# Kernel optimization log

Measured on AMD Instinct MI355X. Metric: run time of the kernel, lower is better.

## Reference

```python
import jax, jax.numpy as jnp
import numpy as np

B, N, C, H, W = 8, 512, 3, 16, 16
K, P, E = 2, 4, 1           # K: hop levels == filter taps, P: attn heads, E: edge feature sets
SLOPE = 0.2                 # LeakyReLU slope in attention
GAT_DIMS = {'d0': (128, 128), 'd1': (512, 32), 'u0': (128, 64),
            'u1': (256, 128), 's0': (128, 128), 's1': (512, 64)}


def _conv(x, w, b):
    pad = w.shape[-1] // 2
    y = jax.lax.conv_general_dilated(x, w, (1, 1), [(pad, pad), (pad, pad)],
                                     dimension_numbers=('NCHW', 'OIHW', 'NCHW'))
    return y + b[None, :, None, None]


def _gat(x, S, wk, wq, wf, b):
    # x: (B,G,N); S: (B,E,N,N) binary GSO. KeyQuery attention + K-tap attentional filter.
    key = jnp.einsum('pegf,bgn->bpefn', wk, x)
    qry = jnp.einsum('pegf,bgn->bpefn', wq, x)
    # scores[...,n,m]: logit of node n attending to neighbor m
    scores = jax.nn.leaky_relu(jnp.einsum('bpefn,bpefm->bpenm', qry, key), SLOPE)
    mask = (jnp.abs(S) > 1e-9)[:, None]                    # (B,1,E,N,N)
    aij = jnp.where(mask, jax.nn.softmax(jnp.where(mask, scores, -1e9), axis=-1), 0.0)
    Pn, En, Kt, G, F = wf.shape
    xk = jnp.broadcast_to(x[:, None, None], (x.shape[0], Pn, En, G, x.shape[-1]))
    zs = [xk]
    for _ in range(Kt - 1):
        xk = jnp.einsum('bpegm,bpenm->bpegn', xk, aij)     # attention-weighted diffusion
        zs.append(xk)
    z = jnp.stack(zs, axis=3)                              # (B,P,E,K,G,N)
    y = jnp.einsum('bpekgn,pekgf->bpfn', z, wf) + b[None, None, :, None]
    y = jax.nn.relu(y)                                     # nonlinearity before head concat
    return y.reshape(y.shape[0], Pn * F, y.shape[-1])      # (B, P*F, N)


def _forward(x, Slist, conv0_w, conv0_b, conv1_w, conv1_b, flat_w, flat_b,
             d0_wk, d0_wq, d0_wf, d0_b, d1_wk, d1_wq, d1_wf, d1_b,
             u0_wk, u0_wq, u0_wf, u0_b, u1_wk, u1_wq, u1_wf, u1_b,
             s0_wk, s0_wq, s0_wf, s0_b, s1_wk, s1_wq, s1_wf, s1_b,
             dec0_w, dec0_b, dec1_w, dec1_b):
    Bn, Nn = x.shape[0], x.shape[1]
    h = x.reshape(Bn * Nn, C, H, W)
    e = jax.nn.relu(_conv(h, conv0_w, conv0_b))
    e = jax.nn.relu(_conv(e, conv1_w, conv1_b))
    e = e + h                                              # RES connection after encoder
    f = jax.nn.relu(e.reshape(Bn * Nn, -1) @ flat_w.T + flat_b)
    g = f.reshape(Bn, -1, Nn)                              # faithful torch reshape to (B, F, N)
    S0, S1 = Slist[:, 0:1], Slist[:, 1:2]
    p0 = g
    p1 = _gat(p0, S0, d0_wk, d0_wq, d0_wf, d0_b)           # downward pass
    p2 = _gat(p1, S1, d1_wk, d1_wq, d1_wf, d1_b)
    # upward pass + shortcuts (upward[l] uses S[K-l-1]; shortcut[K-1-l] on p[K-1-l])
    u0 = _gat(p2, S1, u0_wk, u0_wq, u0_wf, u0_b) + _gat(p1, S1, s1_wk, s1_wq, s1_wf, s1_b)
    u1 = _gat(u0, S0, u1_wk, u1_wq, u1_wf, u1_b) + _gat(p0, S0, s0_wk, s0_wq, s0_wf, s0_b)
    d = jax.nn.relu(u1.reshape(Bn * Nn, -1) @ dec0_w.T + dec0_b)
    out = jax.nn.softmax(d @ dec1_w.T + dec1_b, axis=-1)   # nn.Softmax() -> dim=1 on 2D input
    return out.reshape(Bn, Nn, -1)


def setup_inputs() -> dict:
    key = jax.random.key(0)
    ks = iter(jax.random.split(key, 64))
    def nrm(shape, s=0.1):
        return jax.random.normal(next(ks), shape, jnp.float32) * s
    x = jax.random.normal(next(ks), (B, N, C, H, W), jnp.float32)
    adj = (jax.random.uniform(next(ks), (B, K, N, N)) < 0.02).astype(jnp.float32)
    Slist = jnp.clip(adj + jnp.eye(N, dtype=jnp.float32)[None, None], 0.0, 1.0)
    inp = {'x': x, 'Slist': Slist,
           'conv0_w': nrm((32, C, 3, 3)), 'conv0_b': nrm((32,)),
           'conv1_w': nrm((C, 32, 3, 3)), 'conv1_b': nrm((C,)),
           'flat_w': nrm((128, C * H * W)), 'flat_b': nrm((128,))}
    for pre, (G, F) in GAT_DIMS.items():
        inp[pre + '_wk'] = nrm((P, E, G, F))
        inp[pre + '_wq'] = nrm((P, E, G, F))
        inp[pre + '_wf'] = nrm((P, E, K, G, F))
        inp[pre + '_b'] = nrm((F,))
    inp.update({'dec0_w': nrm((256, 512)), 'dec0_b': nrm((256,)),
                'dec1_w': nrm((5, 256)), 'dec1_b': nrm((5,))})
    return inp


def reference(x, Slist, conv0_w, conv0_b, conv1_w, conv1_b, flat_w, flat_b,
              d0_wk, d0_wq, d0_wf, d0_b, d1_wk, d1_wq, d1_wf, d1_b,
              u0_wk, u0_wq, u0_wf, u0_b, u1_wk, u1_wq, u1_wf, u1_b,
              s0_wk, s0_wq, s0_wf, s0_b, s1_wk, s1_wq, s1_wf, s1_b,
              dec0_w, dec0_b, dec1_w, dec1_b):
    return _forward(x, Slist, conv0_w, conv0_b, conv1_w, conv1_b, flat_w, flat_b,
                    d0_wk, d0_wq, d0_wf, d0_b, d1_wk, d1_wq, d1_wf, d1_b,
                    u0_wk, u0_wq, u0_wf, u0_b, u1_wk, u1_wq, u1_wf, u1_b,
                    s0_wk, s0_wq, s0_wf, s0_b, s1_wk, s1_wq, s1_wf, s1_b,
                    dec0_w, dec0_b, dec1_w, dec1_b)
```

## Files before the change

### kernel.cpp

```cpp
#include <hip/hip_runtime.h>
#include <hip/hip_bf16.h>
#include <math.h>

typedef unsigned short u16;
typedef unsigned int   u32;

#define CAP 48

__device__ __forceinline__ float tof(u16 u){
  union { u32 i; float f; } v; v.i = ((u32)u) << 16; return v.f;
}
__device__ __forceinline__ u16 fromf(float f){
  union { float f; u32 i; } v; v.f = f;
  u32 x = v.i;
  return (u16)((x + 0x7fffu + ((x >> 16) & 1u)) >> 16);
}

__global__ void detect_dtype(const void* xp, int* flag){
  if(threadIdx.x == 0 && blockIdx.x == 0){
    const u16* p = (const u16*)xp;
    int outl = 0;
    for(int i = 0; i < 128; i++){
      u16 u = p[2*i];
      int e = (u >> 7) & 0xFF;
      if(u != 0 && (e < 100 || e > 140)) outl++;
    }
    *flag = (outl > 32) ? 1 : 0;
  }
}

struct WArgs {
  const void* p[34];
  int sz[34];
  int off[35];
};

__global__ __launch_bounds__(256) void convert_weights(WArgs wa, const int* flag,
                                                       float* __restrict__ arena, int total){
  int i = blockIdx.x * 256 + threadIdx.x;
  if(i >= total) return;
  int isf = *flag;
  int t = 0;
  while(wa.off[t+1] <= i) t++;
  int j = i - wa.off[t];
  float v = 0.f;
  if(j < wa.sz[t])
    v = isf ? ((const float*)wa.p[t])[j] : tof(((const u16*)wa.p[t])[j]);
  arena[i] = v;
}

__global__ __launch_bounds__(256) void transpose_w(const float* __restrict__ src,
                                                   float* __restrict__ dst, int R, int C){
  int i = blockIdx.x * 256 + threadIdx.x;
  if(i < R*C){
    int r = i / C, c = i - r*C;
    dst[(size_t)c*R + r] = src[i];
  }
}

__global__ __launch_bounds__(64) void build_nbr(const void* __restrict__ S,
                                                int* __restrict__ nbr_idx,
                                                int* __restrict__ nbr_cnt,
                                                const int* __restrict__ flag){
  int isf = *flag;
  int row  = blockIdx.x;
  int lane = threadIdx.x;
  int cnt = 0;
  for(int c = 0; c < 8; c++){
    int m = c*64 + lane;
    size_t idx = (size_t)row * 512 + m;
    float sv = isf ? ((const float*)S)[idx] : tof(((const u16*)S)[idx]);
    bool pred = fabsf(sv) > 1e-9f;
    unsigned long long mask = __ballot(pred);
    int pos = cnt + __popcll(mask & ((1ull << lane) - 1ull));
    if(pred && pos < CAP) nbr_idx[(size_t)row*CAP + pos] = m;
    cnt += __popcll(mask);
  }
  if(lane == 0) nbr_cnt[row] = cnt > CAP ? CAP : cnt;
}

__global__ __launch_bounds__(256) void encoder_conv(
    const void* __restrict__ x, const int* __restrict__ flag,
    const float* __restrict__ w0, const float* __restrict__ b0,
    const float* __restrict__ w1, const float* __restrict__ b1,
    float* __restrict__ e1n)
{
  __shared__ float xpad[3][18][18];
  __shared__ float e0p[16][18][18];

  int isf = *flag;
  int tid = threadIdx.x;
  size_t img = blockIdx.x;
  int py = tid >> 4, px = tid & 15;

  float* z1 = &xpad[0][0][0];
  for(int i = tid; i < 972; i += 256) z1[i] = 0.f;
  float* z2 = &e0p[0][0][0];
  for(int i = tid; i < 5184; i += 256) z2[i] = 0.f;
  __syncthreads();

  #pragma unroll
  for(int i = 0; i < 3; i++){
    size_t gi = img*768 + i*256 + tid;
    xpad[i][1+py][1+px] = isf ? ((const float*)x)[gi] : tof(((const u16*)x)[gi]);
  }
  __syncthreads();

  float acc1[3] = {0.f, 0.f, 0.f};

  for(int grp = 0; grp < 2; grp++){
    float acc0[16];
    #pragma unroll
    for(int o = 0; o < 16; o++) acc0[o] = 0.f;
    for(int i = 0; i < 3; i++){
      float rr[9];
      #pragma unroll
      for(int ky = 0; ky < 3; ky++)
        #pragma unroll
        for(int kx = 0; kx < 3; kx++)
          rr[ky*3+kx] = xpad[i][py+ky][px+kx];
      #pragma unroll
      for(int o = 0; o < 16; o++){
        #pragma unroll
        for(int t = 0; t < 9; t++)
          acc0[o] = fmaf(rr[t], w0[(grp*16+o)*27 + i*9 + t], acc0[o]);
      }
    }
    __syncthreads();
    #pragma unroll
    for(int o = 0; o < 16; o++)
      e0p[o][1+py][1+px] = fmaxf(acc0[o] + b0[grp*16 + o], 0.f);
    __syncthreads();

    for(int i = 0; i < 16; i++){
      float rr[9];
      #pragma unroll
      for(int ky = 0; ky < 3; ky++)
        #pragma unroll
        for(int kx = 0; kx < 3; kx++)
          rr[ky*3+kx] = e0p[i][py+ky][px+kx];
      int ic = grp*16 + i;
      #pragma unroll
      for(int o = 0; o < 3; o++){
        #pragma unroll
        for(int t = 0; t < 9; t++)
          acc1[o] = fmaf(rr[t], w1[o*288 + ic*9 + t], acc1[o]);
      }
    }
  }

  #pragma unroll
  for(int o = 0; o < 3; o++)
    e1n[img*768 + o*256 + tid] = fmaxf(acc1[o] + b1[o], 0.f) + xpad[o][1+py][1+px];
}

__global__ __launch_bounds__(256) void gemm_flat(
    const float* __restrict__ e1n, const float* __restrict__ fwT,
    const float* __restrict__ fb, float* __restrict__ g)
{
  __shared__ float As[16][68];
  __shared__ float Bs[16][68];
  int tid = threadIdx.x;
  int n0 = blockIdx.x * 64, m0 = blockIdx.y * 64;

  int lk = tid >> 4;
  int l4 = (tid & 15) * 4;
  int br = tid >> 2;
  int bc = (tid & 3) * 4;

  float acc[4][4];
  #pragma unroll
  for(int i = 0; i < 4; i++)
    #pragma unroll
    for(int jj = 0; jj < 4; jj++) acc[i][jj] = 0.f;

  int tm = tid >> 4, tn = tid & 15;
  for(int kt = 0; kt < 48; kt++){
    int k0 = kt*16;
    *(float4*)&As[lk][l4] = *(const float4*)&fwT[(size_t)(k0 + lk)*128 + m0 + l4];
    float4 bv = *(const float4*)&e1n[(size_t)(n0 + br)*768 + k0 + bc];
    Bs[bc+0][br] = bv.x; Bs[bc+1][br] = bv.y; Bs[bc+2][br] = bv.z; Bs[bc+3][br] = bv.w;
    __syncthreads();
    #pragma unroll
    for(int kk = 0; kk < 16; kk++){
      float4 a  = *(const float4*)&As[kk][tm*4];
      float4 xx = *(const float4*)&Bs[kk][tn*4];
      float av[4]  = {a.x, a.y, a.z, a.w};
      float xvv[4] = {xx.x, xx.y, xx.z, xx.w};
      #pragma unroll
      for(int i = 0; i < 4; i++)
        #pragma unroll
        for(int jj = 0; jj < 4; jj++)
          acc[i][jj] = fmaf(av[i], xvv[jj], acc[i][jj]);
    }
    __syncthreads();
  }

  #pragma unroll
  for(int jj = 0; jj < 4; jj++){
    int img = n0 + tn*4 + jj;
    float4 r = make_float4(fmaxf(acc[0][jj] + fb[m0+tm*4+0], 0.f),
                           fmaxf(acc[1][jj] + fb[m0+tm*4+1], 0.f),
                           fmaxf(acc[2][jj] + fb[m0+tm*4+2], 0.f),
                           fmaxf(acc[3][jj] + fb[m0+tm*4+3], 0.f));
    *(float4*)&g[(size_t)img*128 + m0 + tm*4] = r;
  }
}

struct KqP { const float* X; const float* wk; const float* wq; float* kqT;
             int G, F, my; };

__global__ __launch_bounds__(256) void gemm_kq2(KqP A, KqP B)
{
  __shared__ float Ws[32*68];
  __shared__ float Xs[32*68];
  int tid = threadIdx.x;
  int by = blockIdx.y;
  KqP P = (by < A.my) ? A : B;
  int lby = (by < A.my) ? by : (by - A.my);
  int bp = blockIdx.z;
  int b = bp >> 2, p = bp & 3;
  int n0 = blockIdx.x * 64, m0 = lby * 64;
  const float* Xb = P.X + (size_t)b * P.G * 512;

  int lk = tid >> 4;
  int l4 = (tid & 15) * 4;

  int mg = m0 + l4;
  int quad = mg / P.F;
  int mq = mg - quad * P.F;
  size_t GF = (size_t)P.G * P.F;
  const float* wb = (quad == 0 ? P.wk : P.wq) + (size_t)p * GF + mq;

  float acc[4][4];
  #pragma unroll
  for(int i = 0; i < 4; i++)
    #pragma unroll
    for(int jj = 0; jj < 4; jj++) acc[i][jj] = 0.f;

  int tm = tid >> 4, tn = tid & 15;
  int KT = P.G / 32;
  for(int kt = 0; kt < KT; kt++){
    int k = kt*32 + lk;
    *(float4*)&Ws[lk*68 + l4]      = *(const float4*)(wb + (size_t)k * P.F);
    *(float4*)&Ws[(lk+16)*68 + l4] = *(const float4*)(wb + (size_t)(k+16) * P.F);
    *(float4*)&Xs[lk*68 + l4]      = *(const float4*)(Xb + (size_t)k * 512 + n0 + l4);
    *(float4*)&Xs[(lk+16)*68 + l4] = *(const float4*)(Xb + (size_t)(k+16) * 512 + n0 + l4);
    __syncthreads();
    #pragma unroll
    for(int kk = 0; kk < 32; kk++){
      float4 a  = *(const float4*)&Ws[kk*68 + tm*4];
      float4 xx = *(const float4*)&Xs[kk*68 + tn*4];
      float av[4]  = {a.x, a.y, a.z, a.w};
      float xvv[4] = {xx.x, xx.y, xx.z, xx.w};
      #pragma unroll
      for(int i = 0; i < 4; i++)
        #pragma unroll
        for(int jj = 0; jj < 4; jj++)
          acc[i][jj] = fmaf(av[i], xvv[jj], acc[i][jj]);
    }
    __syncthreads();
  }

  int F2 = 2*P.F;
  float* ob = P.kqT + (size_t)bp * 512 * F2;
  #pragma unroll
  for(int jj = 0; jj < 4; jj++){
    float* orow = ob + (size_t)(n0 + tn*4 + jj) * F2 + m0 + tm*4;
    #pragma unroll
    for(int i = 0; i < 4; i++) orow[i] = acc[i][jj];
  }
}

__global__ __launch_bounds__(256) void gemm_kqK64(
    const float* __restrict__ X,
    const float* __restrict__ wk, const float* __restrict__ wq,
    float* __restrict__ kqT, int G, int F)
{
  __shared__ float Ws[64][68];
  __shared__ float Xs[64][68];
  int tid = threadIdx.x;
  int bp = blockIdx.z;
  int b = bp >> 2, p = bp & 3;
  int n0 = blockIdx.x * 64, m0 = blockIdx.y * 64;
  const float* Xb = X + (size_t)b * G * 512;

  int lk = tid >> 4;
  int l4 = (tid & 15) * 4;

  int mg = m0 + l4;
  int quad = mg / F;
  int mq = mg - quad * F;
  size_t GF = (size_t)G * F;
  const float* wb = (quad == 0 ? wk : wq) + (size_t)p * GF + mq;

  float acc[4][4];
  #pragma unroll
  for(int i = 0; i < 4; i++)
    #pragma unroll
    for(int jj = 0; jj < 4; jj++) acc[i][jj] = 0.f;

  int tm = tid >> 4, tn = tid & 15;
  int KT = G / 64;
  for(int kt = 0; kt < KT; kt++){
    #pragma unroll
    for(int kb = 0; kb < 4; kb++){
      int k = kt*64 + lk + kb*16;
      *(float4*)&Ws[lk + kb*16][l4] = *(const float4*)(wb + (size_t)k * F);
      *(float4*)&Xs[lk + kb*16][l4] = *(const float4*)(Xb + (size_t)k * 512 + n0 + l4);
    }
    __syncthreads();
    #pragma unroll
    for(int kk = 0; kk < 64; kk++){
      float4 a  = *(const float4*)&Ws[kk][tm*4];
      float4 xx = *(const float4*)&Xs[kk][tn*4];
      float av[4]  = {a.x, a.y, a.z, a.w};
      float xvv[4] = {xx.x, xx.y, xx.z, xx.w};
      #pragma unroll
      for(int i = 0; i < 4; i++)
        #pragma unroll
        for(int jj = 0; jj < 4; jj++)
          acc[i][jj] = fmaf(av[i], xvv[jj], acc[i][jj]);
    }
    __syncthreads();
  }

  int F2 = 2*F;
  float* ob = kqT + (size_t)bp * 512 * F2;
  #pragma unroll
  for(int jj = 0; jj < 4; jj++){
    float* orow = ob + (size_t)(n0 + tn*4 + jj) * F2 + m0 + tm*4;
    #pragma unroll
    for(int i = 0; i < 4; i++) orow[i] = acc[i][jj];
  }
}

struct AtP { const float* kqT; float* aijv; int F, s; };

__global__ __launch_bounds__(256) void attn2(
    AtP A, AtP B,
    const int* __restrict__ nbr_idx, const int* __restrict__ nbr_cnt)
{
  __shared__ float qs[16][132];
  __shared__ float sc[16][CAP];
  __shared__ float red[16][2];
  int tid = threadIdx.x;
  int n0 = blockIdx.x * 16;
  int bp = blockIdx.y;
  AtP P = (blockIdx.z == 0) ? A : B;
  int b = bp >> 2;
  int F = P.F;
  int F2 = 2*F;
  const float* kqT = P.kqT;

  int F4 = F >> 2;
  for(int i = tid; i < 16*F4; i += 256){
    int r = i / F4, c4 = (i - r*F4) * 4;
    *(float4*)&qs[r][c4] =
      *(const float4*)&kqT[((size_t)bp*512 + n0 + r)*F2 + F + c4];
  }
  __syncthreads();

  int r = tid >> 4;
  int t = tid & 15;
  int n = n0 + r;
  int srow = (b*2 + P.s)*512 + n;
  int cnt = nbr_cnt[srow];
  const int* il = nbr_idx + (size_t)srow * CAP;

  for(int j = t; j < cnt; j += 16){
    int m = il[j];
    const float* krow = kqT + ((size_t)bp*512 + m)*F2;
    float a = 0.f;
    for(int f = 0; f < F; f += 4){
      float4 k4 = *(const float4*)&krow[f];
      a = fmaf(qs[r][f],   k4.x, a);
      a = fmaf(qs[r][f+1], k4.y, a);
      a = fmaf(qs[r][f+2], k4.z, a);
      a = fmaf(qs[r][f+3], k4.w, a);
    }
    sc[r][j] = a >= 0.f ? a : 0.2f * a;
  }
  __syncthreads();

  if(t == 0){
    float mx = -1e30f;
    for(int j = 0; j < cnt; j++) mx = fmaxf(mx, sc[r][j]);
    float ssum = 0.f;
    for(int j = 0; j < cnt; j++) ssum += expf(sc[r][j] - mx);
    red[r][0] = mx; red[r][1] = ssum;
  }
  __syncthreads();

  float mx = red[r][0], ssum = red[r][1];
  float* arow = P.aijv + ((size_t)bp*512 + n)*CAP;
  for(int j = t; j < cnt; j += 16)
    arow[j] = expf(sc[r][j] - mx) / ssum;
}

struct FiP { const float* X; const float* aijv; float* Xp; int G, s, gy; };

__global__ __launch_bounds__(256) void fill_Xp2(
    FiP A, FiP B,
    const int* __restrict__ nbr_idx, const int* __restrict__ nbr_cnt)
{
  __shared__ float xrows[8][512];
  __shared__ float av_s[64][CAP+1];
  __shared__ u16   il_s[64][CAP+2];
  __shared__ int   cnt_s[64];

  int tid = threadIdx.x;
  int by = blockIdx.y;
  FiP P = (by < A.gy) ? A : B;
  int lby = (by < A.gy) ? by : (by - A.gy);
  int n0 = blockIdx.x * 64;
  int g0 = lby * 32;
  int bp = blockIdx.z;
  int b = bp >> 2;
  int srow0 = (b*2 + P.s)*512 + n0;

  for(int i = tid; i < 64*CAP; i += 256){
    int r = i / CAP, j = i - r*CAP;
    il_s[r][j] = (u16)nbr_idx[(size_t)(srow0 + r)*CAP + j];
    av_s[r][j] = P.aijv[((size_t)bp*512 + n0 + r)*CAP + j];
  }
  if(tid < 64) cnt_s[tid] = nbr_cnt[srow0 + tid];

  int n_l = tid & 63;
  int gs  = tid >> 6;
  const float* Xb  = P.X  + ((size_t)b  * P.G + g0) * 512;
  float*       XpB = P.Xp + ((size_t)bp * P.G + g0) * 512;

  for(int gb = 0; gb < 32; gb += 8){
    __syncthreads();
    for(int i = tid; i < 8*128; i += 256){
      int gr = i >> 7, c4 = (i & 127) * 4;
      *(float4*)&xrows[gr][c4] = *(const float4*)&Xb[(size_t)(gb + gr)*512 + c4];
    }
    __syncthreads();
    int cnt = cnt_s[n_l];
    float a0 = 0.f, a1 = 0.f;
    for(int j = 0; j < cnt; j++){
      float w = av_s[n_l][j];
      int   m = il_s[n_l][j];
      a0 = fmaf(w, xrows[gs][m],     a0);
      a1 = fmaf(w, xrows[gs + 4][m], a1);
    }
    XpB[(size_t)(gb + gs)*512     + n0 + n_l] = a0;
    XpB[(size_t)(gb + gs + 4)*512 + n0 + n_l] = a1;
  }
}

struct YP { const float* X; const float* Xp; const float* wf; const float* bias;
            float* out; int G, F, PF, acc, my; };

__global__ __launch_bounds__(256) void gemm_y2_32(YP A, YP B)
{
  __shared__ float Ws[32*68];
  __shared__ float Xs[32*68];
  int tid = threadIdx.x;
  int by = blockIdx.y;
  YP P = (by < A.my) ? A : B;
  int lby = (by < A.my) ? by : (by - A.my);
  int bp = blockIdx.z;
  int b = bp >> 2, p = bp & 3;
  int n0 = blockIdx.x * 64, m0 = lby * 64;
  int G = P.G, F = P.F;

  int lk = tid >> 4;
  int l4 = (tid & 15) * 4;
  int mg = m0 + l4;
  int fcl = mg < F ? mg : (F - 4);
  size_t GF2 = (size_t)2 * G * F;
  const float* wb = P.wf + (size_t)p * GF2 + fcl;

  float acc[4][4];
  #pragma unroll
  for(int i = 0; i < 4; i++)
    #pragma unroll
    for(int jj = 0; jj < 4; jj++) acc[i][jj] = 0.f;

  int tm = tid >> 4, tn = tid & 15;
  int KT = (2*G) / 32;
  for(int kt = 0; kt < KT; kt++){
    int c0 = kt*32 + lk;
    int c1 = c0 + 16;
    const float* xr0 = (c0 < G) ? (P.X  + ((size_t)b  * G + c0      ) * 512)
                                : (P.Xp + ((size_t)bp * G + (c0 - G)) * 512);
    const float* xr1 = (c1 < G) ? (P.X  + ((size_t)b  * G + c1      ) * 512)
                                : (P.Xp + ((size_t)bp * G + (c1 - G)) * 512);
    *(float4*)&Ws[lk*68 + l4]      = *(const float4*)(wb + (size_t)c0 * F);
    *(float4*)&Ws[(lk+16)*68 + l4] = *(const float4*)(wb + (size_t)c1 * F);
    *(float4*)&Xs[lk*68 + l4]      = *(const float4*)(xr0 + n0 + l4);
    *(float4*)&Xs[(lk+16)*68 + l4] = *(const float4*)(xr1 + n0 + l4);
    __syncthreads();
    #pragma unroll
    for(int kk = 0; kk < 32; kk++){
      float4 a  = *(const float4*)&Ws[kk*68 + tm*4];
      float4 xx = *(const float4*)&Xs[kk*68 + tn*4];
      float av[4]  = {a.x, a.y, a.z, a.w};
      float xvv[4] = {xx.x, xx.y, xx.z, xx.w};
      #pragma unroll
      for(int i = 0; i < 4; i++)
        #pragma unroll
        for(int jj = 0; jj < 4; jj++)
          acc[i][jj] = fmaf(av[i], xvv[jj], acc[i][jj]);
    }
    __syncthreads();
  }

  int mrow = m0 + tm*4;
  if(mrow < F){
    float* ob = P.out + ((size_t)b * P.PF + (size_t)p * F + mrow) * 512 + n0 + tn*4;
    #pragma unroll
    for(int i = 0; i < 4; i++){
      float bv = P.bias[mrow + i];
      float4 r = make_float4(fmaxf(acc[i][0] + bv, 0.f),
                             fmaxf(acc[i][1] + bv, 0.f),
                             fmaxf(acc[i][2] + bv, 0.f),
                             fmaxf(acc[i][3] + bv, 0.f));
      float* dst = ob + (size_t)i * 512;
      if(P.acc){
        float4 old = *(float4*)dst;
        r.x += old.x; r.y += old.y; r.z += old.z; r.w += old.w;
      }
      *(float4*)dst = r;
    }
  }
}

__global__ __launch_bounds__(256) void gemm_y2_K64(YP A, YP B)
{
  __shared__ float Ws[64*68];
  __shared__ float Xs[64*68];
  int tid = threadIdx.x;
  int by = blockIdx.y;
  YP P = (by < A.my) ? A : B;
  int lby = (by < A.my) ? by : (by - A.my);
  int bp = blockIdx.z;
  int b = bp >> 2, p = bp & 3;
  int n0 = blockIdx.x * 64, m0 = lby * 64;
  int G = P.G, F = P.F;

  int lk = tid >> 4;
  int l4 = (tid & 15) * 4;
  int mg = m0 + l4;
  int fcl = mg < F ? mg : (F - 4);
  size_t GF2 = (size_t)2 * G * F;
  const float* wb = P.wf + (size_t)p * GF2 + fcl;

  float acc[4][4];
  #pragma unroll
  for(int i = 0; i < 4; i++)
    #pragma unroll
    for(int jj = 0; jj < 4; jj++) acc[i][jj] = 0.f;

  int tm = tid >> 4, tn = tid & 15;
  int KT = (2*G) / 64;
  for(int kt = 0; kt < KT; kt++){
    #pragma unroll
    for(int kb = 0; kb < 4; kb++){
      int c = kt*64 + lk + kb*16;
      const float* xr = (c < G) ? (P.X  + ((size_t)b  * G + c      ) * 512)
                                : (P.Xp + ((size_t)bp * G + (c - G)) * 512);
      *(float4*)&Ws[(lk + kb*16)*68 + l4] = *(const float4*)(wb + (size_t)c * F);
      *(float4*)&Xs[(lk + kb*16)*68 + l4] = *(const float4*)(xr + n0 + l4);
    }
    __syncthreads();
    #pragma unroll
    for(int kk = 0; kk < 64; kk++){
      float4 a  = *(const float4*)&Ws[kk*68 + tm*4];
      float4 xx = *(const float4*)&Xs[kk*68 + tn*4];
      float av[4]  = {a.x, a.y, a.z, a.w};
      float xvv[4] = {xx.x, xx.y, xx.z, xx.w};
      #pragma unroll
      for(int i = 0; i < 4; i++)
        #pragma unroll
        for(int jj = 0; jj < 4; jj++)
          acc[i][jj] = fmaf(av[i], xvv[jj], acc[i][jj]);
    }
    __syncthreads();
  }

  int mrow = m0 + tm*4;
  if(mrow < F){
    float* ob = P.out + ((size_t)b * P.PF + (size_t)p * F + mrow) * 512 + n0 + tn*4;
    #pragma unroll
    for(int i = 0; i < 4; i++){
      float bv = P.bias[mrow + i];
      float4 r = make_float4(fmaxf(acc[i][0] + bv, 0.f),
                             fmaxf(acc[i][1] + bv, 0.f),
                             fmaxf(acc[i][2] + bv, 0.f),
                             fmaxf(acc[i][3] + bv, 0.f));
      float* dst = ob + (size_t)i * 512;
      if(P.acc){
        float4 old = *(float4*)dst;
        r.x += old.x; r.y += old.y; r.z += old.z; r.w += old.w;
      }
      *(float4*)dst = r;
    }
  }
}

__global__ __launch_bounds__(256) void add_vec(float* __restrict__ dst,
                                               const float* __restrict__ src, int n4){
  int i = blockIdx.x * 256 + threadIdx.x;
  if(i < n4){
    float4 a = ((const float4*)dst)[i];
    float4 b = ((const float4*)src)[i];
    a.x += b.x; a.y += b.y; a.z += b.z; a.w += b.w;
    ((float4*)dst)[i] = a;
  }
}

__global__ __launch_bounds__(256) void gemm_dec0(
    const float* __restrict__ u1, const float* __restrict__ w0T,
    const float* __restrict__ b0, float* __restrict__ d)
{
  __shared__ float As[16][68];
  __shared__ float Bs[16][68];
  int tid = threadIdx.x;
  int n0 = blockIdx.x * 64;
  int m0 = blockIdx.y * 64;

  int lk = tid >> 4;
  int l4 = (tid & 15) * 4;
  int br = tid >> 2;
  int bc = (tid & 3) * 4;

  float acc[4][4];
  #pragma unroll
  for(int i = 0; i < 4; i++)
    #pragma unroll
    for(int jj = 0; jj < 4; jj++) acc[i][jj] = 0.f;

  int tm = tid >> 4, tn = tid & 15;
  for(int kt = 0; kt < 32; kt++){
    int k0 = kt*16;
    *(float4*)&As[lk][l4] = *(const float4*)&w0T[(size_t)(k0 + lk)*256 + m0 + l4];
    float4 bv = *(const float4*)&u1[(size_t)(n0 + br)*512 + k0 + bc];
    Bs[bc+0][br] = bv.x; Bs[bc+1][br] = bv.y; Bs[bc+2][br] = bv.z; Bs[bc+3][br] = bv.w;
    __syncthreads();
    #pragma unroll
    for(int kk = 0; kk < 16; kk++){
      float4 a  = *(const float4*)&As[kk][tm*4];
      float4 xx = *(const float4*)&Bs[kk][tn*4];
      float av[4]  = {a.x, a.y, a.z, a.w};
      float xvv[4] = {xx.x, xx.y, xx.z, xx.w};
      #pragma unroll
      for(int i = 0; i < 4; i++)
        #pragma unroll
        for(int jj = 0; jj < 4; jj++)
          acc[i][jj] = fmaf(av[i], xvv[jj], acc[i][jj]);
    }
    __syncthreads();
  }

  #pragma unroll
  for(int jj = 0; jj < 4; jj++){
    int row = n0 + tn*4 + jj;
    float4 r = make_float4(fmaxf(acc[0][jj] + b0[m0+tm*4+0], 0.f),
                           fmaxf(acc[1][jj] + b0[m0+tm*4+1], 0.f),
                           fmaxf(acc[2][jj] + b0[m0+tm*4+2], 0.f),
                           fmaxf(acc[3][jj] + b0[m0+tm*4+3], 0.f));
    *(float4*)&d[(size_t)row*256 + m0 + tm*4] = r;
  }
}

__global__ __launch_bounds__(64) void decoder2(
    const float* __restrict__ d,
    const float* __restrict__ w1, const float* __restrict__ b1,
    const int* __restrict__ flag, void* __restrict__ outp)
{
  __shared__ float ds[256];
  __shared__ float lg[5];
  int r = blockIdx.x, lane = threadIdx.x;
  for(int i = lane; i < 256; i += 64) ds[i] = d[(size_t)r*256 + i];
  __syncthreads();

  if(lane < 5){
    float a = 0.f;
    const float* wr = w1 + (size_t)lane * 256;
    for(int i = 0; i < 256; i++) a = fmaf(ds[i], wr[i], a);
    lg[lane] = a + b1[lane];
  }
  __syncthreads();
  if(lane < 5){
    float mx = lg[0];
    for(int i = 1; i < 5; i++) mx = fmaxf(mx, lg[i]);
    float ssum = 0.f;
    for(int i = 0; i < 5; i++) ssum += expf(lg[i] - mx);
    float v = expf(lg[lane] - mx) / ssum;
    if(*flag) ((float*)outp)[(size_t)r*5 + lane] = v;
    else      ((u16*)outp)[(size_t)r*5 + lane] = fromf(v);
  }
}

extern "C" void kernel_launch(void* const* d_in, const int* in_sizes, int n_in,
                              void* d_out, int out_size, void* d_ws, size_t ws_size,
                              hipStream_t stream)
{
  (void)n_in; (void)out_size; (void)ws_size;
  const void* x = d_in[0];
  const void* S = d_in[1];

  float* wsf   = (float*)d_ws;
  int*   flag  = (int*)d_ws;
  float* arena = wsf + 1024;

  WArgs wa;
  long long aoff[35]; aoff[0] = 0;
  for(int t = 0; t < 34; t++){
    wa.p[t]  = d_in[2 + t];
    wa.sz[t] = in_sizes[2 + t];
    wa.off[t] = (int)aoff[t];
    aoff[t+1] = aoff[t] + ((in_sizes[2 + t] + 15) & ~15);
  }
  wa.off[34] = (int)aoff[34];
  int total = (int)aoff[34];

  size_t cur = 1024 + (size_t)((total + 1023) & ~1023);
  float* g    = wsf + cur; cur += 524288;
  float* p1   = wsf + cur; cur += 2097152;
  float* p2   = wsf + cur; cur += 524288;
  float* u0b  = wsf + cur; cur += 1048576;
  float* u0c  = wsf + cur; cur += 1048576;
  float* u1c  = wsf + cur; cur += 2097152;
  float* u1b  = p1;
  float* aijvA= wsf + cur; cur += (size_t)32*512*CAP;
  float* aijvB= wsf + cur; cur += (size_t)32*512*CAP;
  float* fwT  = wsf + cur; cur += 98304;
  float* dw0T = wsf + cur; cur += 131072;
  int*   ncnt = (int*)(wsf + cur); cur += 8192;
  int*   nidx = (int*)(wsf + cur); cur += (size_t)8192 * CAP;
  float* pool = wsf + cur; cur += 10485760;

  float* e1n   = pool;
  float* kqT0  = pool;
  float* Xp0   = pool;
  float* kqT1  = pool;
  float* Xp1   = pool;
  float* kqT2  = pool;
  float* kqT3  = pool + 2097152;
  float* Xp2   = pool;
  float* Xp3   = pool + 2097152;
  float* kqT4  = pool;
  float* kqT5  = pool + 4194304;
  float* Xp4   = pool;
  float* Xp5   = pool + 4194304;
  float* dbuf  = pool;

  const float* A[34];
  for(int t = 0; t < 34; t++) A[t] = arena + aoff[t];
  const float* c0w = A[0], *c0b = A[1], *c1w = A[2], *c1b = A[3];
  const float* fw  = A[4], *fb  = A[5];
  const float *wk_[6], *wq_[6], *wf_[6], *bias_[6];
  for(int l = 0; l < 6; l++){
    wk_[l]   = A[6 + 4*l];
    wq_[l]   = A[7 + 4*l];
    wf_[l]   = A[8 + 4*l];
    bias_[l] = A[9 + 4*l];
  }
  const float* dw0 = A[30], *db0 = A[31], *dw1 = A[32], *db1 = A[33];

  detect_dtype<<<1, 64, 0, stream>>>(x, flag);
  convert_weights<<<(total + 255)/256, 256, 0, stream>>>(wa, flag, arena, total);
  transpose_w<<<(98304 + 255)/256, 256, 0, stream>>>(fw, fwT, 128, 768);
  transpose_w<<<(131072 + 255)/256, 256, 0, stream>>>(dw0, dw0T, 256, 512);
  build_nbr<<<8192, 64, 0, stream>>>(S, nidx, ncnt, flag);
  encoder_conv<<<4096, 256, 0, stream>>>(x, flag, c0w, c0b, c1w, c1b, e1n);
  gemm_flat<<<dim3(64, 2), 256, 0, stream>>>(e1n, fwT, fb, g);

  {
    KqP k0 = { g, wk_[0], wq_[0], kqT0, 128, 128, 4 };
    gemm_kq2<<<dim3(8, 4, 32), 256, 0, stream>>>(k0, k0);
    AtP a0 = { kqT0, aijvA, 128, 0 };
    attn2<<<dim3(32, 32, 1), 256, 0, stream>>>(a0, a0, nidx, ncnt);
    FiP f0 = { g, aijvA, Xp0, 128, 0, 4 };
    fill_Xp2<<<dim3(8, 4, 32), 256, 0, stream>>>(f0, f0, nidx, ncnt);
    YP y0 = { g, Xp0, wf_[0], bias_[0], p1, 128, 128, 512, 0, 2 };
    gemm_y2_32<<<dim3(8, 2, 32), 256, 0, stream>>>(y0, y0);
  }

  {
    gemm_kqK64<<<dim3(8, 1, 32), 256, 0, stream>>>(p1, wk_[1], wq_[1], kqT1, 512, 32);
    AtP a1 = { kqT1, aijvA, 32, 1 };
    attn2<<<dim3(32, 32, 1), 256, 0, stream>>>(a1, a1, nidx, ncnt);
    FiP f1 = { p1, aijvA, Xp1, 512, 1, 16 };
    fill_Xp2<<<dim3(8, 16, 32), 256, 0, stream>>>(f1, f1, nidx, ncnt);
    YP y1 = { p1, Xp1, wf_[1], bias_[1], p2, 512, 32, 128, 0, 1 };
    gemm_y2_K64<<<dim3(8, 1, 32), 256, 0, stream>>>(y1, y1);
  }

  {
    KqP k2 = { p2, wk_[2], wq_[2], kqT2, 128, 64, 2 };
    KqP k3 = { p1, wk_[5], wq_[5], kqT3, 512, 64, 2 };
    gemm_kq2<<<dim3(8, 4, 32), 256, 0, stream>>>(k2, k3);
    AtP a2 = { kqT2, aijvA, 64, 1 };
    AtP a3 = { kqT3, aijvB, 64, 1 };
    attn2<<<dim3(32, 32, 2), 256, 0, stream>>>(a2, a3, nidx, ncnt);
    FiP f2 = { p2, aijvA, Xp2, 128, 1, 4 };
    FiP f3 = { p1, aijvB, Xp3, 512, 1, 16 };
    fill_Xp2<<<dim3(8, 20, 32), 256, 0, stream>>>(f2, f3, nidx, ncnt);
    YP y2 = { p2, Xp2, wf_[2], bias_[2], u0b, 128, 64, 256, 0, 1 };
    YP y3 = { p1, Xp3, wf_[5], bias_[5], u0c, 512, 64, 256, 0, 1 };
    gemm_y2_K64<<<dim3(8, 2, 32), 256, 0, stream>>>(y2, y3);
    add_vec<<<1024, 256, 0, stream>>>(u0b, u0c, 262144);
  }

  {
    KqP k4 = { u0b, wk_[3], wq_[3], kqT4, 256, 128, 4 };
    KqP k5 = { g,   wk_[4], wq_[4], kqT5, 128, 128, 4 };
    gemm_kq2<<<dim3(8, 8, 32), 256, 0, stream>>>(k4, k5);
    AtP a4 = { kqT4, aijvA, 128, 0 };
    AtP a5 = { kqT5, aijvB, 128, 0 };
    attn2<<<dim3(32, 32, 2), 256, 0, stream>>>(a4, a5, nidx, ncnt);
    FiP f4 = { u0b, aijvA, Xp4, 256, 0, 8 };
    FiP f5 = { g,   aijvB, Xp5, 128, 0, 4 };
    fill_Xp2<<<dim3(8, 12, 32), 256, 0, stream>>>(f4, f5, nidx, ncnt);
    YP y4 = { u0b, Xp4, wf_[3], bias_[3], u1b, 256, 128, 512, 0, 2 };
    YP y5 = { g,   Xp5, wf_[4], bias_[4], u1c, 128, 128, 512, 0, 2 };
    gemm_y2_32<<<dim3(8, 4, 32), 256, 0, stream>>>(y4, y5);
    add_vec<<<2048, 256, 0, stream>>>(u1b, u1c, 524288);
  }

  gemm_dec0<<<dim3(64, 4), 256, 0, stream>>>(u1b, dw0T, db0, dbuf);
  decoder2<<<4096, 64, 0, stream>>>(dbuf, dw1, db1, flag, d_out);
}
```

Baseline: 961.2 us.

## Restructure sparse neighbor gather to map lanes over feature rows

The sparse attention-diffusion kernel now gives each group of 16 lanes one node, with every lane handling a different feature row. Neighbor weights and indices are interleaved in one shared control array, so the lanes of a node read the same entries as broadcasts. The per-block feature tile shrinks from 32 to 16 rows and is loaded once with padded rows, which doubles the grid. Results are staged in shared memory so the global writes are float4 and coalesced. The cost is more blocks that reload the same control data, plus lanes idling up to the largest neighbor count in the wavefront.

Result: slower. 1.302 ms (+35.5%).

```diff
diff --git a/kernel.cpp b/kernel.cpp
--- a/kernel.cpp
+++ b/kernel.cpp
@@ -400,13 +400,13 @@
 
 struct FiP { const float* X; const float* aijv; float* Xp; int G, s, gy; };
 
-__global__ __launch_bounds__(256) void fill_Xp2(
+__global__ __launch_bounds__(256) void fill_Xp3(
     FiP A, FiP B,
     const int* __restrict__ nbr_idx, const int* __restrict__ nbr_cnt)
 {
-  __shared__ float xrows[8][512];
-  __shared__ float av_s[64][CAP+1];
-  __shared__ u16   il_s[64][CAP+2];
+  __shared__ float xrows[16*514];
+  __shared__ u32   ctrl[64*98];
+  __shared__ float out_s[16*68];
   __shared__ int   cnt_s[64];
 
   int tid = threadIdx.x;
@@ -414,40 +414,67 @@
   FiP P = (by < A.gy) ? A : B;
   int lby = (by < A.gy) ? by : (by - A.gy);
   int n0 = blockIdx.x * 64;
-  int g0 = lby * 32;
+  int g0 = lby * 16;
   int bp = blockIdx.z;
   int b = bp >> 2;
   int srow0 = (b*2 + P.s)*512 + n0;
 
   for(int i = tid; i < 64*CAP; i += 256){
     int r = i / CAP, j = i - r*CAP;
-    il_s[r][j] = (u16)nbr_idx[(size_t)(srow0 + r)*CAP + j];
-    av_s[r][j] = P.aijv[((size_t)bp*512 + n0 + r)*CAP + j];
+    u32 wb = __float_as_uint(P.aijv[((size_t)bp*512 + n0 + r)*CAP + j]);
+    u32 mm = (u32)nbr_idx[(size_t)(srow0 + r)*CAP + j];
+    ctrl[r*98 + 2*j]     = wb;
+    ctrl[r*98 + 2*j + 1] = mm;
   }
   if(tid < 64) cnt_s[tid] = nbr_cnt[srow0 + tid];
 
-  int n_l = tid & 63;
-  int gs  = tid >> 6;
-  const float* Xb  = P.X  + ((size_t)b  * P.G + g0) * 512;
-  float*       XpB = P.Xp + ((size_t)bp * P.G + g0) * 512;
-
-  for(int gb = 0; gb < 32; gb += 8){
-    __syncthreads();
-    for(int i = tid; i < 8*128; i += 256){
-      int gr = i >> 7, c4 = (i & 127) * 4;
-      *(float4*)&xrows[gr][c4] = *(const float4*)&Xb[(size_t)(gb + gr)*512 + c4];
-    }
-    __syncthreads();
+  const float* Xb = P.X + ((size_t)b * P.G + g0) * 512;
+  for(int i = tid; i < 16*256; i += 256){
+    int gr = i >> 8, c2 = (i & 255) * 2;
+    float2 v = *(const float2*)&Xb[(size_t)gr*512 + c2];
+    *(float2*)&xrows[gr*514 + c2] = v;
+  }
+  __syncthreads();
+
+  int g_l  = tid & 15;
+  int slot = (tid >> 4) & 3;
+  int wv   = tid >> 6;
+
+  const float* xg = &xrows[g_l*514];
+
+  for(int it = 0; it < 4; it++){
+    int n_l = wv*16 + it*4 + slot;
     int cnt = cnt_s[n_l];
-    float a0 = 0.f, a1 = 0.f;
-    for(int j = 0; j < cnt; j++){
-      float w = av_s[n_l][j];
-      int   m = il_s[n_l][j];
-      a0 = fmaf(w, xrows[gs][m],     a0);
-      a1 = fmaf(w, xrows[gs + 4][m], a1);
-    }
-    XpB[(size_t)(gb + gs)*512     + n0 + n_l] = a0;
-    XpB[(size_t)(gb + gs + 4)*512 + n0 + n_l] = a1;
+    int jmax = cnt;
+    jmax = max(jmax, __shfl_xor(jmax, 16));
+    jmax = max(jmax, __shfl_xor(jmax, 32));
+    const u32* cn = &ctrl[n_l*98];
+    float acc = 0.f;
+    int j = 0;
+    for(; j + 2 <= jmax; j += 2){
+      u32 w0b = cn[2*j],   m0 = cn[2*j+1] & 511u;
+      u32 w1b = cn[2*j+2], m1 = cn[2*j+3] & 511u;
+      float w0 = (j   < cnt) ? __uint_as_float(w0b) : 0.f;
+      float w1 = (j+1 < cnt) ? __uint_as_float(w1b) : 0.f;
+      float x0 = xg[m0];
+      float x1 = xg[m1];
+      acc = fmaf(w0, x0, acc);
+      acc = fmaf(w1, x1, acc);
+    }
+    if(j < jmax){
+      u32 w0b = cn[2*j]; u32 m0 = cn[2*j+1] & 511u;
+      float w0 = (j < cnt) ? __uint_as_float(w0b) : 0.f;
+      acc = fmaf(w0, xg[m0], acc);
+    }
+    out_s[g_l*68 + n_l] = acc;
+  }
+  __syncthreads();
+
+  float* XpB = P.Xp + ((size_t)bp * P.G + g0) * 512;
+  {
+    int gr = tid >> 4, c4 = (tid & 15) * 4;
+    float4 v = *(float4*)&out_s[gr*68 + c4];
+    *(float4*)&XpB[(size_t)gr*512 + n0 + c4] = v;
   }
 }
 
@@ -776,8 +803,8 @@
     gemm_kq2<<<dim3(8, 4, 32), 256, 0, stream>>>(k0, k0);
     AtP a0 = { kqT0, aijvA, 128, 0 };
     attn2<<<dim3(32, 32, 1), 256, 0, stream>>>(a0, a0, nidx, ncnt);
-    FiP f0 = { g, aijvA, Xp0, 128, 0, 4 };
-    fill_Xp2<<<dim3(8, 4, 32), 256, 0, stream>>>(f0, f0, nidx, ncnt);
+    FiP f0 = { g, aijvA, Xp0, 128, 0, 8 };
+    fill_Xp3<<<dim3(8, 8, 32), 256, 0, stream>>>(f0, f0, nidx, ncnt);
     YP y0 = { g, Xp0, wf_[0], bias_[0], p1, 128, 128, 512, 0, 2 };
     gemm_y2_32<<<dim3(8, 2, 32), 256, 0, stream>>>(y0, y0);
   }
@@ -786,8 +813,8 @@
     gemm_kqK64<<<dim3(8, 1, 32), 256, 0, stream>>>(p1, wk_[1], wq_[1], kqT1, 512, 32);
     AtP a1 = { kqT1, aijvA, 32, 1 };
     attn2<<<dim3(32, 32, 1), 256, 0, stream>>>(a1, a1, nidx, ncnt);
-    FiP f1 = { p1, aijvA, Xp1, 512, 1, 16 };
-    fill_Xp2<<<dim3(8, 16, 32), 256, 0, stream>>>(f1, f1, nidx, ncnt);
+    FiP f1 = { p1, aijvA, Xp1, 512, 1, 32 };
+    fill_Xp3<<<dim3(8, 32, 32), 256, 0, stream>>>(f1, f1, nidx, ncnt);
     YP y1 = { p1, Xp1, wf_[1], bias_[1], p2, 512, 32, 128, 0, 1 };
     gemm_y2_K64<<<dim3(8, 1, 32), 256, 0, stream>>>(y1, y1);
   }
@@ -799,9 +826,9 @@
     AtP a2 = { kqT2, aijvA, 64, 1 };
     AtP a3 = { kqT3, aijvB, 64, 1 };
     attn2<<<dim3(32, 32, 2), 256, 0, stream>>>(a2, a3, nidx, ncnt);
-    FiP f2 = { p2, aijvA, Xp2, 128, 1, 4 };
-    FiP f3 = { p1, aijvB, Xp3, 512, 1, 16 };
-    fill_Xp2<<<dim3(8, 20, 32), 256, 0, stream>>>(f2, f3, nidx, ncnt);
+    FiP f2 = { p2, aijvA, Xp2, 128, 1, 8 };
+    FiP f3 = { p1, aijvB, Xp3, 512, 1, 32 };
+    fill_Xp3<<<dim3(8, 40, 32), 256, 0, stream>>>(f2, f3, nidx, ncnt);
     YP y2 = { p2, Xp2, wf_[2], bias_[2], u0b, 128, 64, 256, 0, 1 };
     YP y3 = { p1, Xp3, wf_[5], bias_[5], u0c, 512, 64, 256, 0, 1 };
     gemm_y2_K64<<<dim3(8, 2, 32), 256, 0, stream>>>(y2, y3);
@@ -815,9 +842,9 @@
     AtP a4 = { kqT4, aijvA, 128, 0 };
     AtP a5 = { kqT5, aijvB, 128, 0 };
     attn2<<<dim3(32, 32, 2), 256, 0, stream>>>(a4, a5, nidx, ncnt);
-    FiP f4 = { u0b, aijvA, Xp4, 256, 0, 8 };
-    FiP f5 = { g,   aijvB, Xp5, 128, 0, 4 };
-    fill_Xp2<<<dim3(8, 12, 32), 256, 0, stream>>>(f4, f5, nidx, ncnt);
+    FiP f4 = { u0b, aijvA, Xp4, 256, 0, 16 };
+    FiP f5 = { g,   aijvB, Xp5, 128, 0, 8 };
+    fill_Xp3<<<dim3(8, 24, 32), 256, 0, stream>>>(f4, f5, nidx, ncnt);
     YP y4 = { u0b, Xp4, wf_[3], bias_[3], u1b, 256, 128, 512, 0, 2 };
     YP y5 = { g,   Xp5, wf_[4], bias_[4], u1c, 128, 128, 512, 0, 2 };
     gemm_y2_32<<<dim3(8, 4, 32), 256, 0, stream>>>(y4, y5);
```

## Pack attention weight and neighbor index into u64 and restructure sparse diffusion

Applied to the files above, without the earlier changes.

The attention kernel now writes each softmax weight together with its neighbor index as a packed 64-bit control word, so the diffusion kernel no longer reloads the separate neighbor index table. The new fill kernel stages 16 feature rows transposed into shared memory (padded stride 18) and has each thread gather four features per neighbor with float2 loads, reading control words straight from global memory. The grid doubles along the feature axis to match the smaller per-block slice. The control buffer doubles in size, and the unrolled loop reads up to three padding entries past the neighbor count (masked to zero weight), which depends on the buffer tail being readable.

Measured after the change: 917.3 us. 1.05x faster.

```diff
diff --git a/kernel.cpp b/kernel.cpp
--- a/kernel.cpp
+++ b/kernel.cpp
@@ -4,6 +4,7 @@
 
 typedef unsigned short u16;
 typedef unsigned int   u32;
+typedef unsigned long long u64;
 
 #define CAP 48
 
@@ -335,7 +336,7 @@
   }
 }
 
-struct AtP { const float* kqT; float* aijv; int F, s; };
+struct AtP { const float* kqT; u64* ctrl; int F, s; };
 
 __global__ __launch_bounds__(256) void attn2(
     AtP A, AtP B,
@@ -393,62 +394,73 @@
   __syncthreads();
 
   float mx = red[r][0], ssum = red[r][1];
-  float* arow = P.aijv + ((size_t)bp*512 + n)*CAP;
-  for(int j = t; j < cnt; j += 16)
-    arow[j] = expf(sc[r][j] - mx) / ssum;
-}
-
-struct FiP { const float* X; const float* aijv; float* Xp; int G, s, gy; };
-
-__global__ __launch_bounds__(256) void fill_Xp2(
-    FiP A, FiP B,
-    const int* __restrict__ nbr_idx, const int* __restrict__ nbr_cnt)
-{
-  __shared__ float xrows[8][512];
-  __shared__ float av_s[64][CAP+1];
-  __shared__ u16   il_s[64][CAP+2];
-  __shared__ int   cnt_s[64];
+  u64* crow = P.ctrl + ((size_t)bp*512 + n)*CAP;
+  for(int j = t; j < cnt; j += 16){
+    float w = expf(sc[r][j] - mx) / ssum;
+    crow[j] = (u64)__float_as_uint(w) | ((u64)(u32)il[j] << 32);
+  }
+}
+
+struct FiP { const float* X; const u64* ctrl; float* Xp; int G, s, gy; };
+
+__global__ __launch_bounds__(256) void fill_Xp4(
+    FiP A, FiP B, const int* __restrict__ nbr_cnt)
+{
+  __shared__ float xi[512*18];
 
   int tid = threadIdx.x;
   int by = blockIdx.y;
   FiP P = (by < A.gy) ? A : B;
   int lby = (by < A.gy) ? by : (by - A.gy);
   int n0 = blockIdx.x * 64;
-  int g0 = lby * 32;
+  int g0 = lby * 16;
   int bp = blockIdx.z;
   int b = bp >> 2;
   int srow0 = (b*2 + P.s)*512 + n0;
 
-  for(int i = tid; i < 64*CAP; i += 256){
-    int r = i / CAP, j = i - r*CAP;
-    il_s[r][j] = (u16)nbr_idx[(size_t)(srow0 + r)*CAP + j];
-    av_s[r][j] = P.aijv[((size_t)bp*512 + n0 + r)*CAP + j];
-  }
-  if(tid < 64) cnt_s[tid] = nbr_cnt[srow0 + tid];
+  const float* Xb = P.X + ((size_t)b * P.G + g0) * 512;
+  for(int i = tid; i < 16*512; i += 256){
+    int gl = i >> 9, m = i & 511;
+    xi[m*18 + gl] = Xb[(size_t)gl*512 + m];
+  }
 
   int n_l = tid & 63;
-  int gs  = tid >> 6;
-  const float* Xb  = P.X  + ((size_t)b  * P.G + g0) * 512;
-  float*       XpB = P.Xp + ((size_t)bp * P.G + g0) * 512;
-
-  for(int gb = 0; gb < 32; gb += 8){
-    __syncthreads();
-    for(int i = tid; i < 8*128; i += 256){
-      int gr = i >> 7, c4 = (i & 127) * 4;
-      *(float4*)&xrows[gr][c4] = *(const float4*)&Xb[(size_t)(gb + gr)*512 + c4];
-    }
-    __syncthreads();
-    int cnt = cnt_s[n_l];
-    float a0 = 0.f, a1 = 0.f;
-    for(int j = 0; j < cnt; j++){
-      float w = av_s[n_l][j];
-      int   m = il_s[n_l][j];
-      a0 = fmaf(w, xrows[gs][m],     a0);
-      a1 = fmaf(w, xrows[gs + 4][m], a1);
-    }
-    XpB[(size_t)(gb + gs)*512     + n0 + n_l] = a0;
-    XpB[(size_t)(gb + gs + 4)*512 + n0 + n_l] = a1;
-  }
+  int q   = tid >> 6;
+  int cnt = nbr_cnt[srow0 + n_l];
+  const u64* cn = P.ctrl + ((size_t)bp*512 + n0 + n_l)*CAP;
+  __syncthreads();
+
+  const float* xq = &xi[4*q];
+  float a0=0.f, a1=0.f, a2=0.f, a3=0.f;
+  for(int j0 = 0; j0 < cnt; j0 += 4){
+    u64 c0 = cn[j0], c1 = cn[j0+1], c2 = cn[j0+2], c3 = cn[j0+3];
+    int m0 = (int)(c0 >> 32) & 511;
+    int m1 = (int)(c1 >> 32) & 511;
+    int m2 = (int)(c2 >> 32) & 511;
+    int m3 = (int)(c3 >> 32) & 511;
+    float w0 = __uint_as_float((u32)c0);
+    float w1 = (j0+1 < cnt) ? __uint_as_float((u32)c1) : 0.f;
+    float w2 = (j0+2 < cnt) ? __uint_as_float((u32)c2) : 0.f;
+    float w3 = (j0+3 < cnt) ? __uint_as_float((u32)c3) : 0.f;
+    float2 g0a = *(const float2*)&xq[m0*18], g0b = *(const float2*)&xq[m0*18 + 2];
+    float2 g1a = *(const float2*)&xq[m1*18], g1b = *(const float2*)&xq[m1*18 + 2];
+    float2 g2a = *(const float2*)&xq[m2*18], g2b = *(const float2*)&xq[m2*18 + 2];
+    float2 g3a = *(const float2*)&xq[m3*18], g3b = *(const float2*)&xq[m3*18 + 2];
+    a0 = fmaf(w0, g0a.x, a0); a1 = fmaf(w0, g0a.y, a1);
+    a2 = fmaf(w0, g0b.x, a2); a3 = fmaf(w0, g0b.y, a3);
+    a0 = fmaf(w1, g1a.x, a0); a1 = fmaf(w1, g1a.y, a1);
+    a2 = fmaf(w1, g1b.x, a2); a3 = fmaf(w1, g1b.y, a3);
+    a0 = fmaf(w2, g2a.x, a0); a1 = fmaf(w2, g2a.y, a1);
+    a2 = fmaf(w2, g2b.x, a2); a3 = fmaf(w2, g2b.y, a3);
+    a0 = fmaf(w3, g3a.x, a0); a1 = fmaf(w3, g3a.y, a1);
+    a2 = fmaf(w3, g3b.x, a2); a3 = fmaf(w3, g3b.y, a3);
+  }
+
+  float* ob = P.Xp + ((size_t)bp * P.G + g0 + 4*q) * 512 + n0 + n_l;
+  ob[0]    = a0;
+  ob[512]  = a1;
+  ob[1024] = a2;
+  ob[1536] = a3;
 }
 
 struct YP { const float* X; const float* Xp; const float* wf; const float* bias;
@@ -727,8 +739,8 @@
   float* u0c  = wsf + cur; cur += 1048576;
   float* u1c  = wsf + cur; cur += 2097152;
   float* u1b  = p1;
-  float* aijvA= wsf + cur; cur += (size_t)32*512*CAP;
-  float* aijvB= wsf + cur; cur += (size_t)32*512*CAP;
+  u64*   ctrlA= (u64*)(wsf + cur); cur += (size_t)32*512*CAP*2;
+  u64*   ctrlB= (u64*)(wsf + cur); cur += (size_t)32*512*CAP*2;
   float* fwT  = wsf + cur; cur += 98304;
   float* dw0T = wsf + cur; cur += 131072;
   int*   ncnt = (int*)(wsf + cur); cur += 8192;
@@ -774,20 +786,20 @@
   {
     KqP k0 = { g, wk_[0], wq_[0], kqT0, 128, 128, 4 };
     gemm_kq2<<<dim3(8, 4, 32), 256, 0, stream>>>(k0, k0);
-    AtP a0 = { kqT0, aijvA, 128, 0 };
+    AtP a0 = { kqT0, ctrlA, 128, 0 };
     attn2<<<dim3(32, 32, 1), 256, 0, stream>>>(a0, a0, nidx, ncnt);
-    FiP f0 = { g, aijvA, Xp0, 128, 0, 4 };
-    fill_Xp2<<<dim3(8, 4, 32), 256, 0, stream>>>(f0, f0, nidx, ncnt);
+    FiP f0 = { g, ctrlA, Xp0, 128, 0, 8 };
+    fill_Xp4<<<dim3(8, 8, 32), 256, 0, stream>>>(f0, f0, ncnt);
     YP y0 = { g, Xp0, wf_[0], bias_[0], p1, 128, 128, 512, 0, 2 };
     gemm_y2_32<<<dim3(8, 2, 32), 256, 0, stream>>>(y0, y0);
   }
 
   {
     gemm_kqK64<<<dim3(8, 1, 32), 256, 0, stream>>>(p1, wk_[1], wq_[1], kqT1, 512, 32);
-    AtP a1 = { kqT1, aijvA, 32, 1 };
+    AtP a1 = { kqT1, ctrlA, 32, 1 };
     attn2<<<dim3(32, 32, 1), 256, 0, stream>>>(a1, a1, nidx, ncnt);
-    FiP f1 = { p1, aijvA, Xp1, 512, 1, 16 };
-    fill_Xp2<<<dim3(8, 16, 32), 256, 0, stream>>>(f1, f1, nidx, ncnt);
+    FiP f1 = { p1, ctrlA, Xp1, 512, 1, 32 };
+    fill_Xp4<<<dim3(8, 32, 32), 256, 0, stream>>>(f1, f1, ncnt);
     YP y1 = { p1, Xp1, wf_[1], bias_[1], p2, 512, 32, 128, 0, 1 };
     gemm_y2_K64<<<dim3(8, 1, 32), 256, 0, stream>>>(y1, y1);
   }
@@ -796,12 +808,12 @@
     KqP k2 = { p2, wk_[2], wq_[2], kqT2, 128, 64, 2 };
     KqP k3 = { p1, wk_[5], wq_[5], kqT3, 512, 64, 2 };
     gemm_kq2<<<dim3(8, 4, 32), 256, 0, stream>>>(k2, k3);
-    AtP a2 = { kqT2, aijvA, 64, 1 };
-    AtP a3 = { kqT3, aijvB, 64, 1 };
+    AtP a2 = { kqT2, ctrlA, 64, 1 };
+    AtP a3 = { kqT3, ctrlB, 64, 1 };
     attn2<<<dim3(32, 32, 2), 256, 0, stream>>>(a2, a3, nidx, ncnt);
-    FiP f2 = { p2, aijvA, Xp2, 128, 1, 4 };
-    FiP f3 = { p1, aijvB, Xp3, 512, 1, 16 };
-    fill_Xp2<<<dim3(8, 20, 32), 256, 0, stream>>>(f2, f3, nidx, ncnt);
+    FiP f2 = { p2, ctrlA, Xp2, 128, 1, 8 };
+    FiP f3 = { p1, ctrlB, Xp3, 512, 1, 32 };
+    fill_Xp4<<<dim3(8, 40, 32), 256, 0, stream>>>(f2, f3, ncnt);
     YP y2 = { p2, Xp2, wf_[2], bias_[2], u0b, 128, 64, 256, 0, 1 };
     YP y3 = { p1, Xp3, wf_[5], bias_[5], u0c, 512, 64, 256, 0, 1 };
     gemm_y2_K64<<<dim3(8, 2, 32), 256, 0, stream>>>(y2, y3);
@@ -812,12 +824,12 @@
     KqP k4 = { u0b, wk_[3], wq_[3], kqT4, 256, 128, 4 };
     KqP k5 = { g,   wk_[4], wq_[4], kqT5, 128, 128, 4 };
     gemm_kq2<<<dim3(8, 8, 32), 256, 0, stream>>>(k4, k5);
-    AtP a4 = { kqT4, aijvA, 128, 0 };
-    AtP a5 = { kqT5, aijvB, 128, 0 };
+    AtP a4 = { kqT4, ctrlA, 128, 0 };
+    AtP a5 = { kqT5, ctrlB, 128, 0 };
     attn2<<<dim3(32, 32, 2), 256, 0, stream>>>(a4, a5, nidx, ncnt);
-    FiP f4 = { u0b, aijvA, Xp4, 256, 0, 8 };
-    FiP f5 = { g,   aijvB, Xp5, 128, 0, 4 };
-    fill_Xp2<<<dim3(8, 12, 32), 256, 0, stream>>>(f4, f5, nidx, ncnt);
+    FiP f4 = { u0b, ctrlA, Xp4, 256, 0, 16 };
+    FiP f5 = { g,   ctrlB, Xp5, 128, 0, 8 };
+    fill_Xp4<<<dim3(8, 24, 32), 256, 0, stream>>>(f4, f5, ncnt);
     YP y4 = { u0b, Xp4, wf_[3], bias_[3], u1b, 256, 128, 512, 0, 2 };
     YP y5 = { g,   Xp5, wf_[4], bias_[4], u1c, 128, 128, 512, 0, 2 };
     gemm_y2_32<<<dim3(8, 4, 32), 256, 0, stream>>>(y4, y5);
```
